# Performance work log

Hardware: AMD Instinct MI355X
Metric: run time of the kernel (lower is better)

Reference implementation:

```python
import jax, jax.numpy as jnp
import numpy as np

SIGMA = 1.0
TEMPERATURE = 1.0
GAMMA = 1.0 / (2.0 * SIGMA ** 2)


def setup_inputs() -> dict:
    key = jax.random.key(0)
    k1, k2 = jax.random.split(key)
    B, N, D = 8, 1024, 128
    features_nc = jax.random.normal(k1, (B, N, D), dtype=jnp.float32)
    features_c = jax.random.normal(k2, (B, N, D), dtype=jnp.float32)
    return {"features_nc": features_nc, "features_c": features_c}


def reference(features_nc, features_c):
    D = features_nc.shape[-1]
    x = features_nc.reshape(-1, D)   # (K, D)
    y = features_c.reshape(-1, D)    # (K, D)
    K = x.shape[0]
    x_sq = jnp.sum(x * x, axis=1, keepdims=True)          # (K, 1)
    y_sq = jnp.sum(y * y, axis=1, keepdims=True)          # (K, 1)
    sq_dist = x_sq + y_sq.T - 2.0 * jnp.matmul(x, y.T)    # (K, K)
    logits = (-GAMMA / TEMPERATURE) * sq_dist
    # cross-entropy with labels = arange(K): mean over rows of -log_softmax diag
    log_probs = jax.nn.log_softmax(logits, axis=-1)
    diag = jnp.diagonal(log_probs)
    loss = -jnp.mean(diag)
    return loss
```

## Files before the change

kernel.cpp:

```cpp
#include <hip/hip_runtime.h>
#include <hip/hip_bf16.h>
#include <math.h>

#define KROWS 8192
#define DDIM  128
#define RT    128
#define CTILE 128
#define NTILES 64
#define NRB   64
#define NC0   8
#define TILEB (CTILE * DDIM * 2)
#define SHIFT 94.0f

static constexpr float LOG2E_F = 1.44269504088896340736f;
static constexpr float LN2_F   = 0.69314718055994530942f;

typedef __attribute__((ext_vector_type(8))) short short8;
typedef __attribute__((ext_vector_type(4))) float float4v;

#if __has_builtin(__builtin_amdgcn_exp2f)
#define EXP2(x) __builtin_amdgcn_exp2f(x)
#else
#define EXP2(x) exp2f(x)
#endif

#define AS1C(p) ((const __attribute__((address_space(1))) void*)(p))
#define AS3(p)  ((__attribute__((address_space(3))) void*)(p))

static __device__ __forceinline__ unsigned short f2bf(float f) {
    __hip_bfloat16 h = __float2bfloat16(f);
    return *reinterpret_cast<unsigned short*>(&h);
}

__global__ __launch_bounds__(256) void prep_kernel(
    const float* __restrict__ x, const float* __restrict__ y,
    unsigned int* __restrict__ xb, unsigned int* __restrict__ yb,
    float* __restrict__ xsq2, float* __restrict__ ysq2,
    float* __restrict__ diagn, float* __restrict__ pl)
{
    const int w = threadIdx.x >> 6, lane = threadIdx.x & 63;
    const int row = blockIdx.x * 4 + w;
    if (blockIdx.x < KROWS / 256) pl[blockIdx.x * 256 + threadIdx.x] = 0.0f;
    const float2 xv = *reinterpret_cast<const float2*>(x + (size_t)row * DDIM + lane * 2);
    const float2 yv = *reinterpret_cast<const float2*>(y + (size_t)row * DDIM + lane * 2);
    xb[(size_t)row * 64 + lane] = (unsigned int)f2bf(xv.x * LOG2E_F)
                                | ((unsigned int)f2bf(xv.y * LOG2E_F) << 16);
    yb[(size_t)row * 64 + lane] = (unsigned int)f2bf(yv.x) | ((unsigned int)f2bf(yv.y) << 16);
    float xx = xv.x * xv.x + xv.y * xv.y;
    float yy = yv.x * yv.x + yv.y * yv.y;
    float xy = xv.x * yv.x + xv.y * yv.y;
    #pragma unroll
    for (int o = 32; o > 0; o >>= 1) {
        xx += __shfl_xor(xx, o, 64);
        yy += __shfl_xor(yy, o, 64);
        xy += __shfl_xor(xy, o, 64);
    }
    if (lane == 0) {
        xsq2[row] = fmaf(-0.5f * xx, LOG2E_F, SHIFT);
        ysq2[row] = -0.5f * yy * LOG2E_F;
        diagn[row] = xy - 0.5f * (xx + yy);
    }
}

#define STAGE(BUF, CT)                                                          \
    {                                                                           \
        const char* g_ = (const char*)yb + (size_t)(CT) * TILEB + gswz;         \
        _Pragma("unroll")                                                       \
        for (int q = 0; q < 8; q++)                                             \
            __builtin_amdgcn_global_load_lds(AS1C(g_ + q * 4096),               \
                                             AS3(&BUF[(q * 256 + t) * 16]), 16, 0, 0); \
    }

#define COMPUTE_TILE(BUF, CT)                                                   \
    {                                                                           \
        float b2[8];                                                            \
        _Pragma("unroll")                                                       \
        for (int ci = 0; ci < 8; ci++) b2[ci] = ysq2[(CT) * CTILE + ci * 16 + lo]; \
        float4v acc[2][8];                                                      \
        _Pragma("unroll")                                                       \
        for (int ri = 0; ri < 2; ri++)                                          \
            _Pragma("unroll")                                                   \
            for (int ci = 0; ci < 8; ci++)                                      \
                acc[ri][ci] = (float4v){a2v[ri * 4 + 0] + b2[ci], a2v[ri * 4 + 1] + b2[ci], \
                                        a2v[ri * 4 + 2] + b2[ci], a2v[ri * 4 + 3] + b2[ci]}; \
        _Pragma("unroll")                                                       \
        for (int kk = 0; kk < 4; kk++) {                                        \
            _Pragma("unroll")                                                   \
            for (int ci = 0; ci < 8; ci++) {                                    \
                short8 b = *reinterpret_cast<const short8*>(&BUF[base_k[kk] + ci * 4096]); \
                acc[0][ci] = __builtin_amdgcn_mfma_f32_16x16x32_bf16(af[0][kk], b, acc[0][ci], 0, 0, 0); \
                acc[1][ci] = __builtin_amdgcn_mfma_f32_16x16x32_bf16(af[1][kk], b, acc[1][ci], 0, 0, 0); \
            }                                                                   \
        }                                                                       \
        _Pragma("unroll")                                                       \
        for (int ri = 0; ri < 2; ri++)                                          \
            _Pragma("unroll")                                                   \
            for (int r = 0; r < 4; r++) {                                       \
                float s_ = 0.0f;                                                \
                _Pragma("unroll")                                               \
                for (int ci = 0; ci < 8; ci++) s_ += EXP2(acc[ri][ci][r]);      \
                sums[ri * 4 + r] += s_;                                         \
            }                                                                   \
    }

__global__ __launch_bounds__(256, 2) void gemm_lse_kernel(
    const unsigned short* __restrict__ xb, const unsigned short* __restrict__ yb,
    const float* __restrict__ xsq2, const float* __restrict__ ysq2,
    float* __restrict__ pl)
{
    __shared__ alignas(16) unsigned char Ys0[TILEB];
    __shared__ alignas(16) unsigned char Ys1[TILEB];

    const int t = threadIdx.x;
    const int w = t >> 6, lane = t & 63, quad = lane >> 4, lo = lane & 15;
    const int rb = (blockIdx.x & (NRB - 1)) * RT;
    const int c0 = blockIdx.x >> 6;

    const int gswz = ((t >> 4) << 8) + (((t & 15) ^ ((t >> 4) & 7)) << 4);

    STAGE(Ys0, c0);

    short8 af[2][4];
    #pragma unroll
    for (int ri = 0; ri < 2; ri++)
        #pragma unroll
        for (int kk = 0; kk < 4; kk++)
            af[ri][kk] = *reinterpret_cast<const short8*>(
                xb + (size_t)(rb + w * 32 + ri * 16 + lo) * DDIM + kk * 32 + quad * 8);

    float a2v[8];
    #pragma unroll
    for (int ri = 0; ri < 2; ri++)
        #pragma unroll
        for (int r = 0; r < 4; r++)
            a2v[ri * 4 + r] = xsq2[rb + w * 32 + ri * 16 + quad * 4 + r];

    int base_k[4];
    #pragma unroll
    for (int kk = 0; kk < 4; kk++)
        base_k[kk] = lo * 256 + ((((kk << 2) + quad) ^ (lo & 7)) << 4);

    float sums[8];
    #pragma unroll
    for (int i = 0; i < 8; i++) sums[i] = 0.0f;

    __syncthreads();

    int ct = c0;
    while (true) {
        const int ct1 = ct + NC0;
        if (ct1 < NTILES) STAGE(Ys1, ct1);
        COMPUTE_TILE(Ys0, ct);
        if (ct1 >= NTILES) break;
        __syncthreads();

        const int ct2 = ct + 2 * NC0;
        if (ct2 < NTILES) STAGE(Ys0, ct2);
        COMPUTE_TILE(Ys1, ct1);
        if (ct2 >= NTILES) break;
        __syncthreads();
        ct = ct2;
    }

    #pragma unroll
    for (int i = 0; i < 8; i++) {
        float s = sums[i];
        s += __shfl_xor(s, 1, 64);
        s += __shfl_xor(s, 2, 64);
        s += __shfl_xor(s, 4, 64);
        s += __shfl_xor(s, 8, 64);
        if (lo == 0) {
            int row = rb + w * 32 + (i >> 2) * 16 + quad * 4 + (i & 3);
            atomicAdd(&pl[row], s);
        }
    }
}

__global__ __launch_bounds__(1024) void finish_kernel(
    const float* __restrict__ pl, const float* __restrict__ diagn,
    float* __restrict__ out)
{
    const int t = threadIdx.x;
    float acc = 0.0f;
    for (int r = t; r < KROWS; r += 1024)
        acc += (log2f(pl[r]) - SHIFT) * LN2_F - diagn[r];
    #pragma unroll
    for (int o = 32; o > 0; o >>= 1) acc += __shfl_down(acc, o, 64);
    __shared__ float ws[16];
    if ((t & 63) == 0) ws[t >> 6] = acc;
    __syncthreads();
    if (t == 0) {
        float s = 0.0f;
        #pragma unroll
        for (int i = 0; i < 16; i++) s += ws[i];
        out[0] = s * (1.0f / KROWS);
    }
}

extern "C" void kernel_launch(void* const* d_in, const int* in_sizes, int n_in,
                              void* d_out, int out_size, void* d_ws, size_t ws_size,
                              hipStream_t stream) {
    const float* x = (const float*)d_in[0];
    const float* y = (const float*)d_in[1];
    float* out = (float*)d_out;

    unsigned short* xb = (unsigned short*)d_ws;
    unsigned short* yb = xb + (size_t)KROWS * DDIM;
    float* xsq2  = (float*)(yb + (size_t)KROWS * DDIM);
    float* ysq2  = xsq2 + KROWS;
    float* diagn = ysq2 + KROWS;
    float* pl    = diagn + KROWS;

    prep_kernel<<<KROWS / 4, 256, 0, stream>>>(x, y, (unsigned int*)xb, (unsigned int*)yb,
                                               xsq2, ysq2, diagn, pl);
    gemm_lse_kernel<<<NRB * NC0, 256, 0, stream>>>(xb, yb, xsq2, ysq2, pl);
    finish_kernel<<<1, 1024, 0, stream>>>(pl, diagn, out);
}
```

Baseline: 88.98 us.

## Replace syncthreads double-buffer loop with explicit vmcnt waits and raw barriers

Restructures the tile loop so each buffer is refilled right after it is consumed, using s_waitcnt vmcnt(8) plus raw s_barrier instead of __syncthreads. This keeps one tile's global-to-LDS loads in flight while the other tile is computed, so the full drain of outstanding memory operations at every barrier goes away. It relies on each STAGE issuing exactly 8 vector memory ops and assumes c0 iterations map to exactly 8 tiles. Miscounting would race.

```diff
diff --git a/kernel.cpp b/kernel.cpp
--- a/kernel.cpp
+++ b/kernel.cpp
@@ -26,6 +26,11 @@
 
 #define AS1C(p) ((const __attribute__((address_space(1))) void*)(p))
 #define AS3(p)  ((__attribute__((address_space(3))) void*)(p))
+
+#define FENCE    asm volatile("" ::: "memory")
+#define RAWBAR   __builtin_amdgcn_s_barrier()
+#define WAITVM8  asm volatile("s_waitcnt vmcnt(8)" ::: "memory")
+#define WAITVM0  asm volatile("s_waitcnt vmcnt(0)" ::: "memory")
 
 static __device__ __forceinline__ unsigned short f2bf(float f) {
     __hip_bfloat16 h = __float2bfloat16(f);
@@ -144,22 +149,35 @@
     #pragma unroll
     for (int i = 0; i < 8; i++) sums[i] = 0.0f;
 
-    __syncthreads();
-
-    int ct = c0;
-    while (true) {
-        const int ct1 = ct + NC0;
-        if (ct1 < NTILES) STAGE(Ys1, ct1);
-        COMPUTE_TILE(Ys0, ct);
-        if (ct1 >= NTILES) break;
-        __syncthreads();
-
-        const int ct2 = ct + 2 * NC0;
-        if (ct2 < NTILES) STAGE(Ys0, ct2);
-        COMPUTE_TILE(Ys1, ct1);
-        if (ct2 >= NTILES) break;
-        __syncthreads();
-        ct = ct2;
+    STAGE(Ys1, c0 + NC0);
+    WAITVM8;
+    RAWBAR; FENCE;
+
+    int ctA = c0;
+    int ctB = c0 + NC0;
+    #pragma unroll 1
+    for (int k = 0; k < 4; ++k) {
+        const bool lastk = (k == 3);
+
+        COMPUTE_TILE(Ys0, ctA);
+        FENCE; RAWBAR;
+        if (!lastk) {
+            STAGE(Ys0, ctA + 2 * NC0);
+            WAITVM8;
+        } else {
+            WAITVM0;
+        }
+        RAWBAR; FENCE;
+
+        COMPUTE_TILE(Ys1, ctB);
+        if (!lastk) {
+            FENCE; RAWBAR;
+            STAGE(Ys1, ctB + 2 * NC0);
+            WAITVM8;
+            RAWBAR; FENCE;
+            ctA += 2 * NC0;
+            ctB += 2 * NC0;
+        }
     }
 
     #pragma unroll
```

New measurement: 88.79 us. Within noise of the previous version (-0.2%).
